# Kernel optimization log

Measured on AMD Instinct MI355X. Metric: run time of the kernel, lower is better.

Reference implementation:

```python
import jax, jax.numpy as jnp
import numpy as np

# nuScenes-scale config: batch 2, 360x360 BEV grid (1440/4), 128 channels,
# 10 classes, 200 proposals, 3x3 NMS kernel, 40k occupied voxels per sample.
B, H, W_GRID, NUM_CLS, NUM_PROP, NMS_K = 2, 360, 360, 10, 200, 3
C = 128
N_PER_B = 40000
NEG_FILL = -1000000.0  # scatter_nd fill value from to_dense()


def _bev_pos():
    # replicates create_2D_grid: coord = (x_index_along_dim1, y_index_along_dim0)
    xs = jnp.arange(H, dtype=jnp.float32)
    ys = jnp.arange(W_GRID, dtype=jnp.float32)
    by, bx = jnp.meshgrid(xs, ys, indexing='ij')  # by[i,j]=i, bx[i,j]=j
    return jnp.stack([bx, by], axis=-1).reshape(-1, 2)  # [H*W, 2]


def setup_inputs() -> dict:
    key = jax.random.key(0)
    ks = jax.random.split(key, 10)
    # unique spatial locations per batch sample (sparse voxel coords)
    flats = [jax.random.permutation(ks[i], H * W_GRID)[:N_PER_B] for i in range(B)]
    flat = jnp.concatenate(flats)
    b = jnp.repeat(jnp.arange(B), N_PER_B)
    indices = jnp.stack([b, flat // W_GRID, flat % W_GRID], axis=1).astype(jnp.int32)
    features = jax.random.normal(ks[4], (B * N_PER_B, C), jnp.float32)
    # heatmap head (pointwise linears standing in for the submconv stack)
    W_hm1 = jax.random.normal(ks[5], (C, C), jnp.float32) * (2.0 / C) ** 0.5
    b_hm1 = jnp.zeros((C,), jnp.float32)
    W_hm2 = jax.random.normal(ks[6], (C, NUM_CLS), jnp.float32) * (2.0 / C) ** 0.5
    b_hm2 = jnp.full((NUM_CLS,), -2.19, jnp.float32)  # fc[-1].bias.fill_(-2.19)
    # class_encoding: nn.Conv1d(num_class, channels, 1)
    W_cls = jax.random.normal(ks[7], (C, NUM_CLS), jnp.float32) * 0.1
    b_cls = jnp.zeros((C,), jnp.float32)
    return dict(features=features, W_hm1=W_hm1, b_hm1=b_hm1, W_hm2=W_hm2,
                b_hm2=b_hm2, W_cls=W_cls, b_cls=b_cls, indices=indices)


def reference(features, W_hm1, b_hm1, W_hm2, b_hm2, W_cls, b_cls, indices):
    bidx, yi, xi = indices[:, 0], indices[:, 1], indices[:, 2]
    HW = H * W_GRID

    # --- x.dense(): scatter voxel features to dense BEV grid (zero fill) ---
    xd = jnp.zeros((B, H, W_GRID, C), features.dtype).at[bidx, yi, xi].set(features)
    x_flat = xd.reshape(B, HW, C).transpose(0, 2, 1)  # [B, C, HW]

    # --- heatmap head (per-voxel) then to_dense() with -1e6 fill ---
    hm = jax.nn.relu(features @ W_hm1 + b_hm1) @ W_hm2 + b_hm2  # [N, NUM_CLS]
    dense_hm = jnp.full((B, H, W_GRID, NUM_CLS), NEG_FILL, hm.dtype)
    dense_hm = dense_hm.at[bidx, yi, xi].set(hm).transpose(0, 3, 1, 2)  # [B,K,H,W]

    heat = jax.nn.sigmoid(dense_hm)  # detached in original

    # --- NMS-kernel peak extraction ---
    pad = NMS_K // 2
    inner = jax.lax.reduce_window(heat, -jnp.inf, jax.lax.max,
                                  (1, 1, NMS_K, NMS_K), (1, 1, 1, 1), 'VALID')
    local_max = jnp.zeros_like(heat).at[:, :, pad:H - pad, pad:W_GRID - pad].set(inner)
    # pedestrian (8) and traffic_cone (9): kernel size 1
    local_max = local_max.at[:, 8].set(heat[:, 8]).at[:, 9].set(heat[:, 9])
    heat = heat * (heat == local_max)
    heat_f = heat.reshape(B, NUM_CLS, HW)

    # --- top-k proposals over (class, location) ---
    _, top = jax.lax.top_k(heat_f.reshape(B, -1), NUM_PROP)  # [B, P]
    cls = top // HW
    idx = top % HW

    # --- gather proposal features + class encoding ---
    qf = jnp.take_along_axis(x_flat, jnp.broadcast_to(idx[:, None, :], (B, C, NUM_PROP)), axis=2)
    onehot = jax.nn.one_hot(cls, NUM_CLS, dtype=qf.dtype)  # [B, P, K]
    qf = qf + jnp.einsum('ck,bpk->bcp', W_cls, onehot) + b_cls[None, :, None]

    # --- proposal positions and heatmap scores ---
    query_pos = _bev_pos()[idx]  # [B, P, 2]
    qhs = jnp.take_along_axis(heat_f, jnp.broadcast_to(idx[:, None, :], (B, NUM_CLS, NUM_PROP)), axis=2)
    return qf, query_pos, qhs, cls
```

## Files before the change

kernel.cpp:

```cpp
#include <hip/hip_runtime.h>

#define HW 129600
#define WG 360
#define HG 360
#define NCLS 10
#define NPROP 200
#define CDIM 128
#define NROWS 80000
#define NB 2
#define NPB (NROWS / NB)
#define SEL_CAP 4096
#define HBINS 4096
#define RPB 64
#define PSTR 12

__device__ __forceinline__ void lds_cp16(float* l, const float* g) {
  __builtin_amdgcn_global_load_lds(
      (const __attribute__((address_space(1))) void*)g,
      (__attribute__((address_space(3))) void*)l, 16, 0, 0);
}

__device__ __forceinline__ float4 fmax4(float4 a, float4 b) {
  float4 r;
  r.x = fmaxf(a.x, b.x);
  r.y = fmaxf(a.y, b.y);
  r.z = fmaxf(a.z, b.z);
  r.w = fmaxf(a.w, b.w);
  return r;
}

__global__ __launch_bounds__(256, 4) void k_head(
    const float* __restrict__ feat, const float* __restrict__ W1,
    const float* __restrict__ b1, const float* __restrict__ W2,
    const float* __restrict__ b2, const int* __restrict__ idxs,
    float* __restrict__ dense_heat, int* __restrict__ rowmap) {
  __shared__ __align__(16) float lds_w[2][16 * 128];
  __shared__ __align__(16) float lds_f[2][RPB * 16];
  __shared__ int lds_b[RPB];
  __shared__ int lds_p[RPB];
  const int tid = threadIdx.x;
  const int row0 = blockIdx.x * RPB;
  const int tc = tid & 31;
  const int tr = tid >> 5;
  const int wv = tid >> 6;
  const int lane = tid & 63;

  auto stage = [&](int kt, int nb) {
#pragma unroll
    for (int c = 0; c < 2; ++c) {
      const int off = (wv * 2 + c) * 256;
      lds_cp16(&lds_w[nb][off], W1 + kt * 2048 + off + lane * 4);
    }
    {
      const int off = wv * 256;
      const int fidx = off + lane * 4;
      const int r = fidx >> 4, kk = fidx & 15;
      lds_cp16(&lds_f[nb][off],
               feat + (size_t)(row0 + r) * CDIM + kt * 16 + kk);
    }
  };

  stage(0, 0);
  if (tid < RPB) {
    int row = row0 + tid;
    int bb = idxs[row * 3 + 0];
    int yy = idxs[row * 3 + 1];
    int xx = idxs[row * 3 + 2];
    lds_b[tid] = bb;
    lds_p[tid] = yy * WG + xx;
    rowmap[(size_t)bb * HW + yy * WG + xx] = row;
  }
  __syncthreads();

  float acc[8][4];
#pragma unroll
  for (int r = 0; r < 8; ++r)
#pragma unroll
    for (int c = 0; c < 4; ++c) acc[r][c] = 0.f;

  for (int kt = 0; kt < 8; ++kt) {
    const int cb = kt & 1;
    if (kt < 7) stage(kt + 1, cb ^ 1);
#pragma unroll
    for (int kg = 0; kg < 4; ++kg) {
      float4 w0 = *(const float4*)(&lds_w[cb][(kg * 4 + 0) * 128 + tc * 4]);
      float4 w1 = *(const float4*)(&lds_w[cb][(kg * 4 + 1) * 128 + tc * 4]);
      float4 w2 = *(const float4*)(&lds_w[cb][(kg * 4 + 2) * 128 + tc * 4]);
      float4 w3 = *(const float4*)(&lds_w[cb][(kg * 4 + 3) * 128 + tc * 4]);
#pragma unroll
      for (int r = 0; r < 8; ++r) {
        float4 fv = *(const float4*)(&lds_f[cb][(tr * 8 + r) * 16 + kg * 4]);
        acc[r][0] = fmaf(fv.x, w0.x, acc[r][0]);
        acc[r][0] = fmaf(fv.y, w1.x, acc[r][0]);
        acc[r][0] = fmaf(fv.z, w2.x, acc[r][0]);
        acc[r][0] = fmaf(fv.w, w3.x, acc[r][0]);
        acc[r][1] = fmaf(fv.x, w0.y, acc[r][1]);
        acc[r][1] = fmaf(fv.y, w1.y, acc[r][1]);
        acc[r][1] = fmaf(fv.z, w2.y, acc[r][1]);
        acc[r][1] = fmaf(fv.w, w3.y, acc[r][1]);
        acc[r][2] = fmaf(fv.x, w0.z, acc[r][2]);
        acc[r][2] = fmaf(fv.y, w1.z, acc[r][2]);
        acc[r][2] = fmaf(fv.z, w2.z, acc[r][2]);
        acc[r][2] = fmaf(fv.w, w3.z, acc[r][2]);
        acc[r][3] = fmaf(fv.x, w0.w, acc[r][3]);
        acc[r][3] = fmaf(fv.y, w1.w, acc[r][3]);
        acc[r][3] = fmaf(fv.z, w2.w, acc[r][3]);
        acc[r][3] = fmaf(fv.w, w3.w, acc[r][3]);
      }
    }
    __syncthreads();
  }

  float* w2t = &lds_f[0][0];
  for (int i = tid; i < CDIM * NCLS; i += 256) {
    int k = i / NCLS, j = i - k * NCLS;
    w2t[j * 128 + k] = W2[i];
  }
  __syncthreads();

  float* hbuf = &lds_w[0][0];
  float4 b1v = *(const float4*)(b1 + tc * 4);
#pragma unroll
  for (int half = 0; half < 2; ++half) {
    if ((tr >> 2) == half) {
      int ltr = tr & 3;
#pragma unroll
      for (int r = 0; r < 8; ++r) {
        float4 h;
        h.x = fmaxf(acc[r][0] + b1v.x, 0.f);
        h.y = fmaxf(acc[r][1] + b1v.y, 0.f);
        h.z = fmaxf(acc[r][2] + b1v.z, 0.f);
        h.w = fmaxf(acc[r][3] + b1v.w, 0.f);
        *(float4*)(hbuf + (ltr * 8 + r) * 128 + tc * 4) = h;
      }
    }
    __syncthreads();
    for (int o = tid; o < 32 * NCLS; o += 256) {
      int r = o / NCLS, j = o - r * NCLS;
      float s = b2[j];
      for (int i4 = 0; i4 < 32; ++i4) {
        int k4 = (i4 + tid) & 31;
        float4 hv = *(const float4*)(hbuf + r * 128 + k4 * 4);
        float4 wv2 = *(const float4*)(w2t + j * 128 + k4 * 4);
        s = fmaf(hv.x, wv2.x, s);
        s = fmaf(hv.y, wv2.y, s);
        s = fmaf(hv.z, wv2.z, s);
        s = fmaf(hv.w, wv2.w, s);
      }
      float heat = 1.0f / (1.0f + expf(-s));
      int gr = half * 32 + r;
      dense_heat[((size_t)lds_b[gr] * HW + lds_p[gr]) * PSTR + j] = heat;
    }
    __syncthreads();
  }
}

__global__ __launch_bounds__(256) void k_hist(
    const float* __restrict__ dense_heat, const int* __restrict__ idxs,
    float* __restrict__ val, unsigned int* __restrict__ hist) {
  __shared__ unsigned int lh[HBINS];
  const int tid = threadIdx.x;
  const int row = blockIdx.x * 256 + tid;
  const int blk_b = (blockIdx.x * 256 >= NPB) ? 1 : 0;
  for (int i = tid; i < HBINS; i += 256) lh[i] = 0;
  __syncthreads();

  float v[10];
  int bb = 0;
  const bool valid = row < NROWS;
  if (valid) {
    bb = (row >= NPB) ? 1 : 0;
    const int y = idxs[row * 3 + 1];
    const int x = idxs[row * 3 + 2];
    const int pos = y * WG + x;
    const float* base = dense_heat + ((size_t)bb * HW + pos) * PSTR;
    const bool interior = (y > 0 && y < HG - 1 && x > 0 && x < WG - 1);
    const int d[8] = {-1, 1, -WG - 1, -WG, -WG + 1, WG - 1, WG, WG + 1};
#pragma unroll
    for (int g = 0; g < 2; ++g) {
      float4 cen = *(const float4*)(base + g * 4);
      if (interior) {
        float4 m = cen;
#pragma unroll
        for (int n = 0; n < 8; ++n)
          m = fmax4(m, *(const float4*)(base + d[n] * PSTR + g * 4));
        v[g * 4 + 0] = (cen.x == m.x) ? cen.x : 0.f;
        v[g * 4 + 1] = (cen.y == m.y) ? cen.y : 0.f;
        v[g * 4 + 2] = (cen.z == m.z) ? cen.z : 0.f;
        v[g * 4 + 3] = (cen.w == m.w) ? cen.w : 0.f;
      } else {
        v[g * 4 + 0] = v[g * 4 + 1] = v[g * 4 + 2] = v[g * 4 + 3] = 0.f;
      }
    }
    float2 c89 = *(const float2*)(base + 8);
    v[8] = c89.x;
    v[9] = c89.y;
    float4 s0 = {v[0], v[1], v[2], v[3]};
    float4 s1 = {v[4], v[5], v[6], v[7]};
    float4 s2 = {v[8], v[9], 0.f, 0.f};
    *(float4*)(val + (size_t)row * PSTR + 0) = s0;
    *(float4*)(val + (size_t)row * PSTR + 4) = s1;
    *(float4*)(val + (size_t)row * PSTR + 8) = s2;
#pragma unroll
    for (int c = 0; c < 10; ++c) {
      if (v[c] > 0.f) {
        unsigned int bin = __float_as_uint(v[c]) >> 18;
        if (bb == blk_b)
          atomicAdd(&lh[bin], 1u);
        else
          atomicAdd(&hist[(size_t)bb * HBINS + bin], 1u);
      }
    }
  }
  __syncthreads();
  unsigned int* gh = hist + (size_t)blk_b * HBINS;
  for (int i = tid; i < HBINS; i += 256) {
    unsigned int c = lh[i];
    if (c) atomicAdd(&gh[i], c);
  }
}

__global__ __launch_bounds__(256) void k_collect(
    const float* __restrict__ val, const int* __restrict__ idxs,
    const unsigned int* __restrict__ hist, unsigned long long* __restrict__ sel,
    int* __restrict__ sel_cnt) {
  __shared__ unsigned int coarse[256];
  __shared__ int sT[2];
  const int tid = threadIdx.x;
  for (int bb = 0; bb < NB; ++bb) {
    const unsigned int* h = hist + (size_t)bb * HBINS;
    unsigned int s = 0;
#pragma unroll
    for (int i = 0; i < HBINS / 256; ++i) s += h[tid * (HBINS / 256) + i];
    coarse[tid] = s;
    __syncthreads();
    if (tid == 0) {
      unsigned int cum = 0;
      int T = 0;
      int ci = 255;
      for (; ci >= 0; --ci) {
        if (cum + coarse[ci] >= NPROP) break;
        cum += coarse[ci];
      }
      if (ci >= 0) {
        int t = 15;
        for (; t > 0; --t) {
          unsigned int c = h[ci * 16 + t];
          if (cum + c >= NPROP) break;
          cum += c;
        }
        T = ci * 16 + t;
      }
      sT[bb] = T;
    }
    __syncthreads();
  }
  const int row = blockIdx.x * 256 + tid;
  const bool valid = row < NROWS;
  const int bb = (valid && row >= NPB) ? 1 : 0;
  const int T = sT[bb];
  float v[12];
  int pos = 0;
  if (valid) {
    *(float4*)(v + 0) = *(const float4*)(val + (size_t)row * PSTR + 0);
    *(float4*)(v + 4) = *(const float4*)(val + (size_t)row * PSTR + 4);
    *(float4*)(v + 8) = *(const float4*)(val + (size_t)row * PSTR + 8);
    pos = idxs[row * 3 + 1] * WG + idxs[row * 3 + 2];
  }
  const int lane = tid & 63;
#pragma unroll
  for (int cl = 0; cl < 10; ++cl) {
    float vv = valid ? v[cl] : 0.f;
    unsigned int bits = __float_as_uint(vv);
    bool pred = (vv > 0.f) && ((int)(bits >> 18) >= T);
    unsigned long long m0 = __ballot(pred && (bb == 0));
    unsigned long long m1 = __ballot(pred && (bb == 1));
    if (pred) {
      unsigned long long mask = bb ? m1 : m0;
      int leader = __ffsll((unsigned long long)mask) - 1;
      int lb = __popcll(mask & ((1ull << lane) - 1ull));
      int base = 0;
      if (lane == leader) base = atomicAdd(&sel_cnt[bb], (int)__popcll(mask));
      base = __shfl(base, leader, 64);
      unsigned int gidx = (unsigned int)cl * HW + (unsigned int)pos;
      unsigned long long key =
          ((unsigned long long)bits << 32) | (unsigned long long)(~gidx);
      int slot = base + lb;
      if (slot < SEL_CAP) sel[(size_t)bb * SEL_CAP + slot] = key;
    }
  }
}

__global__ __launch_bounds__(256) void k_final(
    const unsigned long long* __restrict__ sel, const int* __restrict__ sel_cnt,
    const float* __restrict__ val, const int* __restrict__ rowmap,
    const float* __restrict__ feat, const float* __restrict__ Wc,
    const float* __restrict__ bc, float* __restrict__ out) {
  __shared__ unsigned long long sk[SEL_CAP];
  __shared__ unsigned long long winners[NPROP];
  __shared__ int wcls[NPROP];
  __shared__ int wrow[NPROP];
  const int b = blockIdx.x;
  const int tid = threadIdx.x;
  int M = sel_cnt[b];
  if (M > SEL_CAP) M = SEL_CAP;
  for (int i = tid; i < M; i += 256) sk[i] = sel[(size_t)b * SEL_CAP + i];
  __syncthreads();
  for (int i = tid; i < M; i += 256) {
    unsigned long long key = sk[i];
    int rank = 0;
    for (int j = 0; j < M; ++j) rank += (sk[j] > key) ? 1 : 0;
    if (rank < NPROP) winners[rank] = key;
  }
  __syncthreads();
  if (tid < NPROP) {
    unsigned long long key = winners[tid];
    unsigned int gidx = ~((unsigned int)(key & 0xFFFFFFFFull));
    int cls = (int)(gidx / HW);
    int pos = (int)(gidx - (unsigned int)cls * HW);
    int y = pos / WG, x = pos - y * WG;
    wcls[tid] = cls;
    wrow[tid] = rowmap[(size_t)b * HW + pos];
    out[51200 + ((size_t)b * NPROP + tid) * 2 + 0] = (float)x;
    out[51200 + ((size_t)b * NPROP + tid) * 2 + 1] = (float)y;
    out[56000 + b * NPROP + tid] = (float)cls;
  }
  __syncthreads();
  for (int o = tid; o < NCLS * NPROP; o += 256) {
    int j = o / NPROP, pp = o - j * NPROP;
    out[52000 + (size_t)b * NCLS * NPROP + o] = val[(size_t)wrow[pp] * PSTR + j];
  }
  for (int o = tid; o < CDIM * NPROP; o += 256) {
    int c = o / NPROP, pp = o - c * NPROP;
    out[(size_t)b * CDIM * NPROP + o] =
        feat[(size_t)wrow[pp] * CDIM + c] + Wc[c * NCLS + wcls[pp]] + bc[c];
  }
}

extern "C" void kernel_launch(void* const* d_in, const int* in_sizes, int n_in,
                              void* d_out, int out_size, void* d_ws,
                              size_t ws_size, hipStream_t stream) {
  const float* feat = (const float*)d_in[0];
  const float* W1 = (const float*)d_in[1];
  const float* b1 = (const float*)d_in[2];
  const float* W2 = (const float*)d_in[3];
  const float* b2 = (const float*)d_in[4];
  const float* Wc = (const float*)d_in[5];
  const float* bc = (const float*)d_in[6];
  const int* idxs = (const int*)d_in[7];
  float* out = (float*)d_out;

  char* ws = (char*)d_ws;
  float* dense_heat = (float*)(ws + 0);
  unsigned int* hist = (unsigned int*)(ws + 12441600);
  int* rowmap = (int*)(ws + 12474368);
  unsigned long long* sel = (unsigned long long*)(ws + 13511168);
  int* sel_cnt = (int*)(ws + 13576704);
  float* val = (float*)(ws + 13576720);

  hipMemsetAsync(dense_heat, 0, (size_t)NB * HW * PSTR * sizeof(float), stream);
  hipMemsetAsync(hist, 0, (size_t)NB * HBINS * sizeof(unsigned int), stream);
  hipMemsetAsync(sel_cnt, 0, 2 * sizeof(int), stream);

  k_head<<<NROWS / RPB, 256, 0, stream>>>(feat, W1, b1, W2, b2, idxs, dense_heat,
                                          rowmap);
  k_hist<<<(NROWS + 255) / 256, 256, 0, stream>>>(dense_heat, idxs, val, hist);
  k_collect<<<(NROWS + 255) / 256, 256, 0, stream>>>(val, idxs, hist, sel,
                                                     sel_cnt);
  k_final<<<NB, 256, 0, stream>>>(sel, sel_cnt, val, rowmap, feat, Wc, bc, out);
}
```

Before: 201.0 us.

## Replace dense heat grid with compact per-row heat and rowmap neighbor lookup

The head kernel now writes heatmap values compactly by voxel row instead of into a dense padded BEV grid. The 3x3 NMS in k_hist finds neighbors through the rowmap index (initialized to -1) and falls back to a zero row when a neighbor is empty. This removes the ~12 MB dense grid memset and the scattered writes into it, and only a 1 MB rowmap fill remains. In exchange each neighbor needs an extra dependent indirect load.

```diff
diff --git a/kernel.cpp b/kernel.cpp
--- a/kernel.cpp
+++ b/kernel.cpp
@@ -33,11 +33,9 @@
     const float* __restrict__ feat, const float* __restrict__ W1,
     const float* __restrict__ b1, const float* __restrict__ W2,
     const float* __restrict__ b2, const int* __restrict__ idxs,
-    float* __restrict__ dense_heat, int* __restrict__ rowmap) {
+    float* __restrict__ val_raw, int* __restrict__ rowmap) {
   __shared__ __align__(16) float lds_w[2][16 * 128];
   __shared__ __align__(16) float lds_f[2][RPB * 16];
-  __shared__ int lds_b[RPB];
-  __shared__ int lds_p[RPB];
   const int tid = threadIdx.x;
   const int row0 = blockIdx.x * RPB;
   const int tc = tid & 31;
@@ -66,8 +64,6 @@
     int bb = idxs[row * 3 + 0];
     int yy = idxs[row * 3 + 1];
     int xx = idxs[row * 3 + 2];
-    lds_b[tid] = bb;
-    lds_p[tid] = yy * WG + xx;
     rowmap[(size_t)bb * HW + yy * WG + xx] = row;
   }
   __syncthreads();
@@ -149,14 +145,15 @@
       }
       float heat = 1.0f / (1.0f + expf(-s));
       int gr = half * 32 + r;
-      dense_heat[((size_t)lds_b[gr] * HW + lds_p[gr]) * PSTR + j] = heat;
+      val_raw[(size_t)(row0 + gr) * PSTR + j] = heat;
     }
     __syncthreads();
   }
 }
 
 __global__ __launch_bounds__(256) void k_hist(
-    const float* __restrict__ dense_heat, const int* __restrict__ idxs,
+    const float* __restrict__ val_raw, const int* __restrict__ idxs,
+    const int* __restrict__ rowmap, const float* __restrict__ zrow,
     float* __restrict__ val, unsigned int* __restrict__ hist) {
   __shared__ unsigned int lh[HBINS];
   const int tid = threadIdx.x;
@@ -173,26 +170,34 @@
     const int y = idxs[row * 3 + 1];
     const int x = idxs[row * 3 + 2];
     const int pos = y * WG + x;
-    const float* base = dense_heat + ((size_t)bb * HW + pos) * PSTR;
+    const float* cbase = val_raw + (size_t)row * PSTR;
+    float4 c0 = *(const float4*)(cbase + 0);
+    float4 c1 = *(const float4*)(cbase + 4);
+    float2 c89 = *(const float2*)(cbase + 8);
     const bool interior = (y > 0 && y < HG - 1 && x > 0 && x < WG - 1);
-    const int d[8] = {-1, 1, -WG - 1, -WG, -WG + 1, WG - 1, WG, WG + 1};
-#pragma unroll
-    for (int g = 0; g < 2; ++g) {
-      float4 cen = *(const float4*)(base + g * 4);
-      if (interior) {
-        float4 m = cen;
-#pragma unroll
-        for (int n = 0; n < 8; ++n)
-          m = fmax4(m, *(const float4*)(base + d[n] * PSTR + g * 4));
-        v[g * 4 + 0] = (cen.x == m.x) ? cen.x : 0.f;
-        v[g * 4 + 1] = (cen.y == m.y) ? cen.y : 0.f;
-        v[g * 4 + 2] = (cen.z == m.z) ? cen.z : 0.f;
-        v[g * 4 + 3] = (cen.w == m.w) ? cen.w : 0.f;
-      } else {
-        v[g * 4 + 0] = v[g * 4 + 1] = v[g * 4 + 2] = v[g * 4 + 3] = 0.f;
-      }
-    }
-    float2 c89 = *(const float2*)(base + 8);
+    if (interior) {
+      const int d[8] = {-1, 1, -WG - 1, -WG, -WG + 1, WG - 1, WG, WG + 1};
+      float4 m0 = c0, m1 = c1;
+      const int* rmb = rowmap + (size_t)bb * HW + pos;
+#pragma unroll
+      for (int n = 0; n < 8; ++n) {
+        int nrow = rmb[d[n]];
+        const float* p =
+            (nrow >= 0) ? (val_raw + (size_t)nrow * PSTR) : zrow;
+        m0 = fmax4(m0, *(const float4*)(p + 0));
+        m1 = fmax4(m1, *(const float4*)(p + 4));
+      }
+      v[0] = (c0.x == m0.x) ? c0.x : 0.f;
+      v[1] = (c0.y == m0.y) ? c0.y : 0.f;
+      v[2] = (c0.z == m0.z) ? c0.z : 0.f;
+      v[3] = (c0.w == m0.w) ? c0.w : 0.f;
+      v[4] = (c1.x == m1.x) ? c1.x : 0.f;
+      v[5] = (c1.y == m1.y) ? c1.y : 0.f;
+      v[6] = (c1.z == m1.z) ? c1.z : 0.f;
+      v[7] = (c1.w == m1.w) ? c1.w : 0.f;
+    } else {
+      v[0] = v[1] = v[2] = v[3] = v[4] = v[5] = v[6] = v[7] = 0.f;
+    }
     v[8] = c89.x;
     v[9] = c89.y;
     float4 s0 = {v[0], v[1], v[2], v[3]};
@@ -351,20 +356,23 @@
   float* out = (float*)d_out;
 
   char* ws = (char*)d_ws;
-  float* dense_heat = (float*)(ws + 0);
-  unsigned int* hist = (unsigned int*)(ws + 12441600);
-  int* rowmap = (int*)(ws + 12474368);
-  unsigned long long* sel = (unsigned long long*)(ws + 13511168);
-  int* sel_cnt = (int*)(ws + 13576704);
-  float* val = (float*)(ws + 13576720);
-
-  hipMemsetAsync(dense_heat, 0, (size_t)NB * HW * PSTR * sizeof(float), stream);
-  hipMemsetAsync(hist, 0, (size_t)NB * HBINS * sizeof(unsigned int), stream);
+  float* zrow = (float*)(ws + 0);
+  unsigned int* hist = (unsigned int*)(ws + 64);
+  int* rowmap = (int*)(ws + 32832);
+  unsigned long long* sel = (unsigned long long*)(ws + 1069632);
+  int* sel_cnt = (int*)(ws + 1135168);
+  float* val_raw = (float*)(ws + 1135184);
+  float* val = (float*)(ws + 4975184);
+
+  hipMemsetAsync(ws, 0, 64 + (size_t)NB * HBINS * sizeof(unsigned int),
+                 stream);
+  hipMemsetAsync(rowmap, 0xFF, (size_t)NB * HW * sizeof(int), stream);
   hipMemsetAsync(sel_cnt, 0, 2 * sizeof(int), stream);
 
-  k_head<<<NROWS / RPB, 256, 0, stream>>>(feat, W1, b1, W2, b2, idxs, dense_heat,
+  k_head<<<NROWS / RPB, 256, 0, stream>>>(feat, W1, b1, W2, b2, idxs, val_raw,
                                           rowmap);
-  k_hist<<<(NROWS + 255) / 256, 256, 0, stream>>>(dense_heat, idxs, val, hist);
+  k_hist<<<(NROWS + 255) / 256, 256, 0, stream>>>(val_raw, idxs, rowmap, zrow,
+                                                  val, hist);
   k_collect<<<(NROWS + 255) / 256, 256, 0, stream>>>(val, idxs, hist, sel,
                                                      sel_cnt);
   k_final<<<NB, 256, 0, stream>>>(sel, sel_cnt, val, rowmap, feat, Wc, bc, out);
```

New measurement: 196.0 us. 2.4% less time.
